# Optimization experiments

Hardware: AMD Instinct MI355X
Metric: run time of the kernel (lower is better)

## Reference

```python
import jax, jax.numpy as jnp
import numpy as np

N_TRACK = 50000
N_LANE = 50000
N_ATT = N_TRACK + N_LANE
NP_T = 1000000
NP_L = 500000
E_ATT = 1600000
D_TRACK = 4
D_LANE = 2
D_ATT = 10
HEADS = 30
D_OUT = 2
EPS = 1e-5
NEG_SLOPE = 0.2


def _mlp(x, W, b, g, beta):
    # Linear -> LayerNorm -> ReLU (matches MLP module)
    h = x @ W + b
    mu = h.mean(-1, keepdims=True)
    var = ((h - mu) ** 2).mean(-1, keepdims=True)
    h = (h - mu) * jax.lax.rsqrt(var + EPS) * g + beta
    return jax.nn.relu(h)


def _seg_max0(x, ids, n):
    # DGL max-reduce; nodes with no in-edges get 0
    m = jax.ops.segment_max(x, ids, num_segments=n, indices_are_sorted=True)
    return jnp.where(jnp.isfinite(m), m, 0.0)


def setup_inputs() -> dict:
    key = jax.random.key(0)
    ks = jax.random.split(key, 16)
    g = lambda i, shape, s=1.0: jax.random.normal(ks[i], shape, jnp.float32) * s
    return {
        'track_point_feats': g(0, (NP_T, D_TRACK)),
        'lane_point_feats': g(1, (NP_L, D_LANE)),
        'point_track_id': jnp.sort(jax.random.randint(ks[2], (NP_T,), 0, N_TRACK)),
        'point_lane_id': jnp.sort(jax.random.randint(ks[3], (NP_L,), 0, N_LANE)),
        'att_src': jax.random.randint(ks[4], (E_ATT,), 0, N_ATT),
        'att_dst': jnp.sort(jax.random.randint(ks[5], (E_ATT,), 0, N_ATT)),
        'track_mlp_W': g(6, (D_TRACK, D_TRACK), 0.5),
        'track_mlp_b': jnp.zeros((D_TRACK,), jnp.float32),
        'track_ln_g': jnp.ones((D_TRACK,), jnp.float32),
        'track_ln_b': jnp.zeros((D_TRACK,), jnp.float32),
        'track_out_W': g(7, (D_TRACK, D_ATT), 0.5),
        'track_out_b': jnp.zeros((D_ATT,), jnp.float32),
        'lane_mlp_W': g(8, (D_LANE, D_LANE), 0.5),
        'lane_mlp_b': jnp.zeros((D_LANE,), jnp.float32),
        'lane_ln_g': jnp.ones((D_LANE,), jnp.float32),
        'lane_ln_b': jnp.zeros((D_LANE,), jnp.float32),
        'lane_out_W': g(9, (D_LANE, D_ATT), 0.5),
        'lane_out_b': jnp.zeros((D_ATT,), jnp.float32),
        'gat_fc_W': g(10, (D_ATT, HEADS * D_OUT), 0.3),
        'gat_attn_l': g(11, (HEADS, D_OUT), 0.3),
        'gat_attn_r': g(12, (HEADS, D_OUT), 0.3),
        'gat_bias': jnp.zeros((HEADS * D_OUT,), jnp.float32),
    }


def reference(track_point_feats, lane_point_feats, point_track_id, point_lane_id,
              att_src, att_dst,
              track_mlp_W, track_mlp_b, track_ln_g, track_ln_b, track_out_W, track_out_b,
              lane_mlp_W, lane_mlp_b, lane_ln_g, lane_ln_b, lane_out_W, lane_out_b,
              gat_fc_W, gat_attn_l, gat_attn_r, gat_bias):
    # SubTrackModel: per-point MLP -> segment max over point->track -> linear
    track_pool = _seg_max0(_mlp(track_point_feats, track_mlp_W, track_mlp_b, track_ln_g, track_ln_b),
                           point_track_id, N_TRACK)
    track_feats = track_pool @ track_out_W + track_out_b  # [N_TRACK, 10]
    # SubLaneModel
    lane_pool = _seg_max0(_mlp(lane_point_feats, lane_mlp_W, lane_mlp_b, lane_ln_g, lane_ln_b),
                          point_lane_id, N_LANE)
    lane_feats = lane_pool @ lane_out_W + lane_out_b  # [N_LANE, 10]
    feats = jnp.concatenate([track_feats, lane_feats], axis=0)  # [N_ATT, 10]

    # GATConv (30 heads, out 2)
    h = (feats @ gat_fc_W).reshape(N_ATT, HEADS, D_OUT)
    el = jnp.einsum('nhd,hd->nh', h, gat_attn_l)
    er = jnp.einsum('nhd,hd->nh', h, gat_attn_r)
    e = jax.nn.leaky_relu(el[att_src] + er[att_dst], NEG_SLOPE)  # [E, H]
    m = jax.ops.segment_max(e, att_dst, num_segments=N_ATT, indices_are_sorted=True)
    m = jnp.where(jnp.isfinite(m), m, 0.0)
    ee = jnp.exp(e - m[att_dst])
    den = jax.ops.segment_sum(ee, att_dst, num_segments=N_ATT, indices_are_sorted=True)
    alpha = ee / den[att_dst]  # edge softmax over incoming edges per dst
    msg = alpha[:, :, None] * h[att_src]  # [E, H, D_OUT]
    out = jax.ops.segment_sum(msg, att_dst, num_segments=N_ATT, indices_are_sorted=True)
    out = out.reshape(N_ATT, HEADS * D_OUT) + gat_bias
    return out[:N_TRACK]
```

## Files before the change

### kernel.cpp

```cpp
#include <hip/hip_runtime.h>
#include <hip/hip_bf16.h>
#include <math.h>

#define N_TRACK 50000
#define N_LANE  50000
#define N_ATT   (N_TRACK + N_LANE)
#define NP_T    1000000
#define NP_L    500000
#define E_ATT   1600000
#define HEADS   30
#define EPS     1e-5f
#define NEG_SLOPE 0.2f

#define REC_DW 32

__global__ void point_kernel(const float4* __restrict__ xt, const float2* __restrict__ xl,
                             const int* __restrict__ idt, const int* __restrict__ idl,
                             const float* __restrict__ tW, const float* __restrict__ tb,
                             const float* __restrict__ tg, const float* __restrict__ tbeta,
                             const float* __restrict__ lW, const float* __restrict__ lb,
                             const float* __restrict__ lg, const float* __restrict__ lbeta,
                             float* __restrict__ pool_t, float* __restrict__ pool_l) {
    int tid = blockIdx.x * blockDim.x + threadIdx.x;
    int lane = threadIdx.x & 63;
    int id = -1;
    float y0 = 0.f, y1 = 0.f, y2 = 0.f, y3 = 0.f;
    if (tid < NP_T) {
        float4 xv = xt[tid];
        float h[4];
        #pragma unroll
        for (int j = 0; j < 4; j++)
            h[j] = xv.x * tW[0*4+j] + xv.y * tW[1*4+j] + xv.z * tW[2*4+j] + xv.w * tW[3*4+j] + tb[j];
        float mu = 0.25f * (h[0] + h[1] + h[2] + h[3]);
        float var = 0.f;
        #pragma unroll
        for (int j = 0; j < 4; j++) { float d = h[j] - mu; var += d * d; }
        var *= 0.25f;
        float r = rsqrtf(var + EPS);
        y0 = fmaxf((h[0] - mu) * r * tg[0] + tbeta[0], 0.f);
        y1 = fmaxf((h[1] - mu) * r * tg[1] + tbeta[1], 0.f);
        y2 = fmaxf((h[2] - mu) * r * tg[2] + tbeta[2], 0.f);
        y3 = fmaxf((h[3] - mu) * r * tg[3] + tbeta[3], 0.f);
        id = idt[tid];
    } else if (tid < NP_T + NP_L) {
        int t = tid - NP_T;
        float2 xv = xl[t];
        float h0 = xv.x * lW[0] + xv.y * lW[2] + lb[0];
        float h1 = xv.x * lW[1] + xv.y * lW[3] + lb[1];
        float mu = 0.5f * (h0 + h1);
        float var = 0.5f * ((h0 - mu) * (h0 - mu) + (h1 - mu) * (h1 - mu));
        float r = rsqrtf(var + EPS);
        y0 = fmaxf((h0 - mu) * r * lg[0] + lbeta[0], 0.f);
        y1 = fmaxf((h1 - mu) * r * lg[1] + lbeta[1], 0.f);
        id = N_TRACK + idl[t];
    }
    #pragma unroll
    for (int d = 1; d < 64; d <<= 1) {
        int oid = __shfl_down(id, d, 64);
        float o0 = __shfl_down(y0, d, 64);
        float o1 = __shfl_down(y1, d, 64);
        float o2 = __shfl_down(y2, d, 64);
        float o3 = __shfl_down(y3, d, 64);
        if (oid == id) {
            y0 = fmaxf(y0, o0); y1 = fmaxf(y1, o1);
            y2 = fmaxf(y2, o2); y3 = fmaxf(y3, o3);
        }
    }
    int pid = __shfl_up(id, 1, 64);
    bool head = (lane == 0) || (pid != id);
    if (id >= 0 && head) {
        if (id < N_TRACK) {
            unsigned int* p = (unsigned int*)&pool_t[(size_t)id * 4];
            atomicMax(p + 0, __float_as_uint(y0));
            atomicMax(p + 1, __float_as_uint(y1));
            atomicMax(p + 2, __float_as_uint(y2));
            atomicMax(p + 3, __float_as_uint(y3));
        } else {
            unsigned int* p = (unsigned int*)&pool_l[(size_t)(id - N_TRACK) * 2];
            atomicMax(p + 0, __float_as_uint(y0));
            atomicMax(p + 1, __float_as_uint(y1));
        }
    }
}

__global__ void node_kernel(const float* __restrict__ pool_t, const float* __restrict__ pool_l,
                            const float* __restrict__ tW, const float* __restrict__ tb,
                            const float* __restrict__ lW, const float* __restrict__ lb,
                            const float* __restrict__ fcW,
                            const int* __restrict__ att_dst,
                            unsigned int* __restrict__ hpack, int* __restrict__ off) {
    int i = blockIdx.x * blockDim.x + threadIdx.x;

    if (i <= N_TRACK) {
        int lo = 0, hi = E_ATT;
        while (lo < hi) {
            int mid = (lo + hi) >> 1;
            if (att_dst[mid] < i) lo = mid + 1; else hi = mid;
        }
        off[i] = lo;
    }
    if (i >= N_ATT) return;

    float f[10];
    if (i < N_TRACK) {
        const float4 p = *(const float4*)(pool_t + (size_t)i * 4);
        #pragma unroll
        for (int j = 0; j < 10; j++)
            f[j] = p.x * tW[0*10+j] + p.y * tW[1*10+j] + p.z * tW[2*10+j] + p.w * tW[3*10+j] + tb[j];
    } else {
        const float2 p = *(const float2*)(pool_l + (size_t)(i - N_TRACK) * 2);
        #pragma unroll
        for (int j = 0; j < 10; j++)
            f[j] = p.x * lW[0*10+j] + p.y * lW[1*10+j] + lb[j];
    }

    unsigned int rec[REC_DW];
    #pragma unroll
    for (int hh = 0; hh < HEADS; hh++) {
        float a0 = 0.f, a1 = 0.f;
        #pragma unroll
        for (int k = 0; k < 10; k++) {
            a0 += f[k] * fcW[k * 60 + 2 * hh];
            a1 += f[k] * fcW[k * 60 + 2 * hh + 1];
        }
        unsigned int b0 = (unsigned int)__hip_bfloat16_raw(__float2bfloat16(a0)).x;
        unsigned int b1 = (unsigned int)__hip_bfloat16_raw(__float2bfloat16(a1)).x;
        rec[hh] = b0 | (b1 << 16);
    }
    rec[30] = 0u; rec[31] = 0u;

    uint4* rp = (uint4*)(hpack + (size_t)i * REC_DW);
    #pragma unroll
    for (int q = 0; q < 8; q++)
        rp[q] = make_uint4(rec[4*q], rec[4*q+1], rec[4*q+2], rec[4*q+3]);
}

__global__ void edge_kernel(const int* __restrict__ src, const int* __restrict__ off,
                            const unsigned int* __restrict__ hpack,
                            const float* __restrict__ attn_l, const float* __restrict__ attn_r,
                            const float* __restrict__ bias, float* __restrict__ out) {
    int grp = blockIdx.x * 8 + (threadIdx.x >> 5);
    int hh = threadIdx.x & 31;
    if (grp >= N_TRACK || hh >= HEADS) return;

    float al0 = attn_l[2 * hh], al1 = attn_l[2 * hh + 1];
    float ar0 = attn_r[2 * hh], ar1 = attn_r[2 * hh + 1];

    unsigned int dd = hpack[(size_t)grp * REC_DW + hh];
    float hd0 = __uint_as_float(dd << 16);
    float hd1 = __uint_as_float(dd & 0xffff0000u);
    float er = hd0 * ar0 + hd1 * ar1;

    int s = off[grp], e = off[grp + 1];
    float m = -INFINITY, den = 0.f, n0 = 0.f, n1 = 0.f;

    for (int kk = s; kk < e; kk += 16) {
        int lim = e - kk;
        int sv[16];
        #pragma unroll
        for (int j = 0; j < 16; j++) sv[j] = src[kk + (j < lim ? j : 0)];
        unsigned int d[16];
        #pragma unroll
        for (int j = 0; j < 16; j++) d[j] = hpack[(size_t)sv[j] * REC_DW + hh];
        #pragma unroll
        for (int j = 0; j < 16; j++) {
            if (j < lim) {
                float h0 = __uint_as_float(d[j] << 16);
                float h1 = __uint_as_float(d[j] & 0xffff0000u);
                float ev = h0 * al0 + h1 * al1 + er;
                ev = (ev > 0.f) ? ev : NEG_SLOPE * ev;
                float nm = fmaxf(m, ev);
                float sc = __expf(m - nm);
                float w  = __expf(ev - nm);
                den = den * sc + w;
                n0  = n0 * sc + w * h0;
                n1  = n1 * sc + w * h1;
                m = nm;
            }
        }
    }

    float o0 = 0.f, o1 = 0.f;
    if (den > 0.f) {
        float inv = 1.f / den;
        o0 = n0 * inv; o1 = n1 * inv;
    }
    ((float2*)out)[(size_t)grp * HEADS + hh] =
        make_float2(o0 + bias[2 * hh], o1 + bias[2 * hh + 1]);
}

extern "C" void kernel_launch(void* const* d_in, const int* in_sizes, int n_in,
                              void* d_out, int out_size, void* d_ws, size_t ws_size,
                              hipStream_t stream) {
    const float4* track_pts = (const float4*)d_in[0];
    const float2* lane_pts  = (const float2*)d_in[1];
    const int* pt_track_id  = (const int*)d_in[2];
    const int* pt_lane_id   = (const int*)d_in[3];
    const int* att_src      = (const int*)d_in[4];
    const int* att_dst      = (const int*)d_in[5];
    const float* track_mlp_W = (const float*)d_in[6];
    const float* track_mlp_b = (const float*)d_in[7];
    const float* track_ln_g  = (const float*)d_in[8];
    const float* track_ln_b  = (const float*)d_in[9];
    const float* track_out_W = (const float*)d_in[10];
    const float* track_out_b = (const float*)d_in[11];
    const float* lane_mlp_W  = (const float*)d_in[12];
    const float* lane_mlp_b  = (const float*)d_in[13];
    const float* lane_ln_g   = (const float*)d_in[14];
    const float* lane_ln_b   = (const float*)d_in[15];
    const float* lane_out_W  = (const float*)d_in[16];
    const float* lane_out_b  = (const float*)d_in[17];
    const float* gat_fc_W    = (const float*)d_in[18];
    const float* gat_attn_l  = (const float*)d_in[19];
    const float* gat_attn_r  = (const float*)d_in[20];
    const float* gat_bias    = (const float*)d_in[21];
    float* out = (float*)d_out;

    float* pool_t = (float*)d_ws;
    float* pool_l = pool_t + 200000;
    int*   off    = (int*)(pool_l + 100000);
    unsigned int* hpack = (unsigned int*)(off + 50016);

    hipMemsetAsync(d_ws, 0, 300000 * sizeof(float), stream);

    point_kernel<<<(NP_T + NP_L + 255) / 256, 256, 0, stream>>>(
        track_pts, lane_pts, pt_track_id, pt_lane_id,
        track_mlp_W, track_mlp_b, track_ln_g, track_ln_b,
        lane_mlp_W, lane_mlp_b, lane_ln_g, lane_ln_b,
        pool_t, pool_l);
    node_kernel<<<(N_ATT + 255) / 256, 256, 0, stream>>>(
        pool_t, pool_l, track_out_W, track_out_b, lane_out_W, lane_out_b,
        gat_fc_W, att_dst, hpack, off);
    edge_kernel<<<(N_TRACK + 7) / 8, 256, 0, stream>>>(
        att_src, off, hpack, gat_attn_l, gat_attn_r, gat_bias, out);
}
```

Measured before the change: 174.0 us.

## Split each destination's edges across two half-waves and merge online-softmax states

The edge kernel now gives each destination node a full 64-lane wave instead of a 32-lane group. Each half-wave handles alternate edges, and the two partial online-softmax states are combined through a cross-half shuffle. This halves the serial per-node edge chain and doubles the gathers in flight, at the cost of twice as many launched threads and a merge step. Point-kernel input loads and the output store also become nontemporal hints to avoid cache pollution.

```diff
diff --git a/kernel.cpp b/kernel.cpp
--- a/kernel.cpp
+++ b/kernel.cpp
@@ -12,9 +12,12 @@
 #define EPS     1e-5f
 #define NEG_SLOPE 0.2f
 
+typedef __attribute__((ext_vector_type(4))) float nfloat4;
+typedef __attribute__((ext_vector_type(2))) float nfloat2;
+
 #define REC_DW 32
 
-__global__ void point_kernel(const float4* __restrict__ xt, const float2* __restrict__ xl,
+__global__ void point_kernel(const nfloat4* __restrict__ xt, const nfloat2* __restrict__ xl,
                              const int* __restrict__ idt, const int* __restrict__ idl,
                              const float* __restrict__ tW, const float* __restrict__ tb,
                              const float* __restrict__ tg, const float* __restrict__ tbeta,
@@ -26,7 +29,7 @@
     int id = -1;
     float y0 = 0.f, y1 = 0.f, y2 = 0.f, y3 = 0.f;
     if (tid < NP_T) {
-        float4 xv = xt[tid];
+        nfloat4 xv = __builtin_nontemporal_load(&xt[tid]);
         float h[4];
         #pragma unroll
         for (int j = 0; j < 4; j++)
@@ -41,10 +44,10 @@
         y1 = fmaxf((h[1] - mu) * r * tg[1] + tbeta[1], 0.f);
         y2 = fmaxf((h[2] - mu) * r * tg[2] + tbeta[2], 0.f);
         y3 = fmaxf((h[3] - mu) * r * tg[3] + tbeta[3], 0.f);
-        id = idt[tid];
+        id = __builtin_nontemporal_load(&idt[tid]);
     } else if (tid < NP_T + NP_L) {
         int t = tid - NP_T;
-        float2 xv = xl[t];
+        nfloat2 xv = __builtin_nontemporal_load(&xl[t]);
         float h0 = xv.x * lW[0] + xv.y * lW[2] + lb[0];
         float h1 = xv.x * lW[1] + xv.y * lW[3] + lb[1];
         float mu = 0.5f * (h0 + h1);
@@ -52,7 +55,7 @@
         float r = rsqrtf(var + EPS);
         y0 = fmaxf((h0 - mu) * r * lg[0] + lbeta[0], 0.f);
         y1 = fmaxf((h1 - mu) * r * lg[1] + lbeta[1], 0.f);
-        id = N_TRACK + idl[t];
+        id = N_TRACK + __builtin_nontemporal_load(&idl[t]);
     }
     #pragma unroll
     for (int d = 1; d < 64; d <<= 1) {
@@ -139,32 +142,35 @@
                             const unsigned int* __restrict__ hpack,
                             const float* __restrict__ attn_l, const float* __restrict__ attn_r,
                             const float* __restrict__ bias, float* __restrict__ out) {
-    int grp = blockIdx.x * 8 + (threadIdx.x >> 5);
-    int hh = threadIdx.x & 31;
-    if (grp >= N_TRACK || hh >= HEADS) return;
-
-    float al0 = attn_l[2 * hh], al1 = attn_l[2 * hh + 1];
-    float ar0 = attn_r[2 * hh], ar1 = attn_r[2 * hh + 1];
-
-    unsigned int dd = hpack[(size_t)grp * REC_DW + hh];
-    float hd0 = __uint_as_float(dd << 16);
-    float hd1 = __uint_as_float(dd & 0xffff0000u);
-    float er = hd0 * ar0 + hd1 * ar1;
-
-    int s = off[grp], e = off[grp + 1];
+    int wave = blockIdx.x * 4 + (threadIdx.x >> 6);
+    int lane = threadIdx.x & 63;
+    int hh = lane & 31;
+    int half = lane >> 5;
+    if (wave >= N_TRACK) return;
+    int hc = (hh < HEADS) ? hh : (HEADS - 1);
+
+    float al0 = attn_l[2 * hc], al1 = attn_l[2 * hc + 1];
+    float ar0 = attn_r[2 * hc], ar1 = attn_r[2 * hc + 1];
+
+    unsigned int dd = hpack[(size_t)wave * REC_DW + hc];
+    float er = __uint_as_float(dd << 16) * ar0 + __uint_as_float(dd & 0xffff0000u) * ar1;
+
+    int s = off[wave], e = off[wave + 1];
     float m = -INFINITY, den = 0.f, n0 = 0.f, n1 = 0.f;
 
-    for (int kk = s; kk < e; kk += 16) {
-        int lim = e - kk;
-        int sv[16];
-        #pragma unroll
-        for (int j = 0; j < 16; j++) sv[j] = src[kk + (j < lim ? j : 0)];
-        unsigned int d[16];
-        #pragma unroll
-        for (int j = 0; j < 16; j++) d[j] = hpack[(size_t)sv[j] * REC_DW + hh];
-        #pragma unroll
-        for (int j = 0; j < 16; j++) {
-            if (j < lim) {
+    for (int kk = s + half; kk < e; kk += 16) {
+        int sv[8];
+        #pragma unroll
+        for (int j = 0; j < 8; j++) {
+            int idx = kk + 2 * j;
+            sv[j] = src[idx < e ? idx : kk];
+        }
+        unsigned int d[8];
+        #pragma unroll
+        for (int j = 0; j < 8; j++) d[j] = hpack[(size_t)sv[j] * REC_DW + hc];
+        #pragma unroll
+        for (int j = 0; j < 8; j++) {
+            if (kk + 2 * j < e) {
                 float h0 = __uint_as_float(d[j] << 16);
                 float h1 = __uint_as_float(d[j] & 0xffff0000u);
                 float ev = h0 * al0 + h1 * al1 + er;
@@ -180,20 +186,35 @@
         }
     }
 
-    float o0 = 0.f, o1 = 0.f;
-    if (den > 0.f) {
-        float inv = 1.f / den;
-        o0 = n0 * inv; o1 = n1 * inv;
-    }
-    ((float2*)out)[(size_t)grp * HEADS + hh] =
-        make_float2(o0 + bias[2 * hh], o1 + bias[2 * hh + 1]);
+    if (e > s) {
+        float mo = __shfl_xor(m, 32, 64);
+        float dn = __shfl_xor(den, 32, 64);
+        float a0 = __shfl_xor(n0, 32, 64);
+        float a1 = __shfl_xor(n1, 32, 64);
+        float nm = fmaxf(m, mo);
+        float sa = (m  > -INFINITY) ? __expf(m  - nm) : 0.f;
+        float sb = (mo > -INFINITY) ? __expf(mo - nm) : 0.f;
+        den = den * sa + dn * sb;
+        n0  = n0 * sa + a0 * sb;
+        n1  = n1 * sa + a1 * sb;
+    }
+
+    if (half == 0 && hh < HEADS) {
+        float o0 = 0.f, o1 = 0.f;
+        if (den > 0.f) {
+            float inv = 1.f / den;
+            o0 = n0 * inv; o1 = n1 * inv;
+        }
+        nfloat2 v = { o0 + bias[2 * hh], o1 + bias[2 * hh + 1] };
+        __builtin_nontemporal_store(v, (nfloat2*)out + (size_t)wave * HEADS + hh);
+    }
 }
 
 extern "C" void kernel_launch(void* const* d_in, const int* in_sizes, int n_in,
                               void* d_out, int out_size, void* d_ws, size_t ws_size,
                               hipStream_t stream) {
-    const float4* track_pts = (const float4*)d_in[0];
-    const float2* lane_pts  = (const float2*)d_in[1];
+    const nfloat4* track_pts = (const nfloat4*)d_in[0];
+    const nfloat2* lane_pts  = (const nfloat2*)d_in[1];
     const int* pt_track_id  = (const int*)d_in[2];
     const int* pt_lane_id   = (const int*)d_in[3];
     const int* att_src      = (const int*)d_in[4];
@@ -221,7 +242,7 @@
     int*   off    = (int*)(pool_l + 100000);
     unsigned int* hpack = (unsigned int*)(off + 50016);
 
-    hipMemsetAsync(d_ws, 0, 300000 * sizeof(float), stream);
+    (void)hipMemsetAsync(d_ws, 0, 300000 * sizeof(float), stream);
 
     point_kernel<<<(NP_T + NP_L + 255) / 256, 256, 0, stream>>>(
         track_pts, lane_pts, pt_track_id, pt_lane_id,
@@ -231,6 +252,6 @@
     node_kernel<<<(N_ATT + 255) / 256, 256, 0, stream>>>(
         pool_t, pool_l, track_out_W, track_out_b, lane_out_W, lane_out_b,
         gat_fc_W, att_dst, hpack, off);
-    edge_kernel<<<(N_TRACK + 7) / 8, 256, 0, stream>>>(
+    edge_kernel<<<(N_TRACK + 3) / 4, 256, 0, stream>>>(
         att_src, off, hpack, gat_attn_l, gat_attn_r, gat_bias, out);
 }
```

Measured after the change: 175.7 us. No clear change (+0.9%).
